# Kernel optimization log

Hardware: AMD Instinct MI355X
Metric: run time of the kernel (lower is better)

The kernel has to match this reference:

```python
import jax, jax.numpy as jnp
import numpy as np

B, N, DIM, H, POS_DIM = 8, 1024, 512, 8, 50
D = DIM // H


def setup_inputs() -> dict:
    key = jax.random.key(0)
    ks = jax.random.split(key, 7)
    s = 0.02
    return {
        "x": jax.random.normal(ks[0], (B, N, DIM), jnp.float32),
        "pos": jax.random.normal(ks[1], (1, N, N, POS_DIM), jnp.float32),
        "W_kv": jax.random.normal(ks[2], (2 * DIM, DIM), jnp.float32) * s,
        "W_out": jax.random.normal(ks[3], (DIM, DIM), jnp.float32) * s,
        "b_out": jax.random.normal(ks[4], (DIM,), jnp.float32) * s,
        "w_pos": jax.random.normal(ks[5], (POS_DIM,), jnp.float32) * s,
        "b_pos": jax.random.normal(ks[6], (1,), jnp.float32) * s,
    }


def reference(x, pos, W_kv, W_out, b_out, w_pos, b_pos):
    b, n, dim = x.shape
    h, d = H, dim // H
    scale = dim ** -0.5
    # to_kv: Linear(dim, 2*dim, bias=False); layout 'b n (kv h d)'
    kv = x @ W_kv.T                                   # (b, n, 2*dim)
    k = kv[..., :dim].reshape(b, n, h, d).transpose(0, 2, 1, 3)   # (b,h,n,d)
    v = kv[..., dim:].reshape(b, n, h, d).transpose(0, 2, 1, 3)   # (b,h,n,d)
    dots = jnp.einsum('bhid,bhjd->bhij', k, k) * scale            # (b,h,n,n)
    # map_pos(dots[...,None] + pos[None]) == dots*sum(w) + pos@w + bias (Linear is linear)
    pos_bias = jnp.einsum('ijp,p->ij', pos[0, :n, :n, :], w_pos)  # (n,n)
    scores = dots * jnp.sum(w_pos) + pos_bias + b_pos[0]
    attn = jax.nn.softmax(scores, axis=-1)
    out = jnp.einsum('bhij,bhjd->bhid', attn, v)                  # (b,h,n,d)
    out = out.transpose(0, 2, 1, 3).reshape(b, n, dim)            # (b,n,dim)
    return out @ W_out.T + b_out
```

## Files before the change

### kernel.cpp

```cpp
#include <hip/hip_runtime.h>

#define B_ 8
#define N_ 1024
#define DIM_ 512
#define H_ 8
#define D_ 64
#define PD_ 50
#define PBROWS 256

typedef __attribute__((ext_vector_type(4))) float f32x4;
typedef __attribute__((ext_vector_type(8))) __bf16 bf16x8;

__device__ __forceinline__ unsigned short f2bf(float f) {
    unsigned int u = __float_as_uint(f);
    u += 0x7FFFu + ((u >> 16) & 1u);
    return (unsigned short)(u >> 16);
}

__global__ __launch_bounds__(256) void cast_all(const float* __restrict__ x,
                                                const float* __restrict__ wkv,
                                                const float* __restrict__ wout,
                                                unsigned short* __restrict__ xb,
                                                unsigned short* __restrict__ wkvb,
                                                unsigned short* __restrict__ woutb) {
    const int bid = blockIdx.x;
    const float* src;
    unsigned short* dst;
    int idx;
    if (bid < 4096)      { src = x;    dst = xb;    idx = bid; }
    else if (bid < 4608) { src = wkv;  dst = wkvb;  idx = bid - 4096; }
    else                 { src = wout; dst = woutb; idx = bid - 4608; }
    int i = idx * 256 + threadIdx.x;
    float4 v = reinterpret_cast<const float4*>(src)[i];
    ushort4 o;
    o.x = f2bf(v.x); o.y = f2bf(v.y); o.z = f2bf(v.z); o.w = f2bf(v.w);
    reinterpret_cast<ushort4*>(dst)[i] = o;
}

__global__ __launch_bounds__(256) void pos_bias_kernel(const float* __restrict__ pos,
                                                       const float* __restrict__ w_pos,
                                                       float* __restrict__ pb) {
    __shared__ float buf[PBROWS * PD_];
    const int t = threadIdx.x;
    const size_t base = (size_t)blockIdx.x * (PBROWS * PD_);
    const float4* src = reinterpret_cast<const float4*>(pos + base);
    float4* dst = reinterpret_cast<float4*>(buf);
#pragma unroll 4
    for (int i = t; i < PBROWS * PD_ / 4; i += 256)
        dst[i] = src[i];
    __syncthreads();
    float acc = 0.f;
    const float* row = buf + t * PD_;
#pragma unroll
    for (int p = 0; p < PD_; p++) acc += row[p] * w_pos[p];
    pb[(size_t)blockIdx.x * PBROWS + t] = acc;
}

__global__ __launch_bounds__(256) void kv_gemm(const unsigned short* __restrict__ xb,
                                               const unsigned short* __restrict__ wb,
                                               unsigned short* __restrict__ kb,
                                               unsigned short* __restrict__ vt) {
    __shared__ __align__(16) unsigned short As[128][40];
    __shared__ __align__(16) unsigned short Bs[64][40];
    const int m0 = blockIdx.x * 128;
    const int n0 = blockIdx.y * 64;
    const int t = threadIdx.x;
    const int w = t >> 6, l = t & 63;
    const int wr = (w >> 1) * 64, wc = (w & 1) * 32;
    const int lr = l & 15, lg = l >> 4;
    const int ar = t >> 1, ac = (t & 1) * 16;
    const int br = t >> 2, bc = (t & 3) * 8;

    f32x4 acc[4][2] = {};

    for (int k0 = 0; k0 < DIM_; k0 += 32) {
        __syncthreads();
        *reinterpret_cast<bf16x8*>(&As[ar][ac]) =
            *reinterpret_cast<const bf16x8*>(&xb[(size_t)(m0 + ar) * DIM_ + k0 + ac]);
        *reinterpret_cast<bf16x8*>(&As[ar][ac + 8]) =
            *reinterpret_cast<const bf16x8*>(&xb[(size_t)(m0 + ar) * DIM_ + k0 + ac + 8]);
        *reinterpret_cast<bf16x8*>(&Bs[br][bc]) =
            *reinterpret_cast<const bf16x8*>(&wb[(size_t)(n0 + br) * DIM_ + k0 + bc]);
        __syncthreads();
        bf16x8 b0 = *reinterpret_cast<const bf16x8*>(&Bs[wc + lr][lg * 8]);
        bf16x8 b1 = *reinterpret_cast<const bf16x8*>(&Bs[wc + 16 + lr][lg * 8]);
#pragma unroll
        for (int fm = 0; fm < 4; fm++) {
            bf16x8 a = *reinterpret_cast<const bf16x8*>(&As[wr + fm * 16 + lr][lg * 8]);
            acc[fm][0] = __builtin_amdgcn_mfma_f32_16x16x32_bf16(a, b0, acc[fm][0], 0, 0, 0);
            acc[fm][1] = __builtin_amdgcn_mfma_f32_16x16x32_bf16(a, b1, acc[fm][1], 0, 0, 0);
        }
    }

#pragma unroll
    for (int fm = 0; fm < 4; fm++)
#pragma unroll
        for (int fn = 0; fn < 2; fn++) {
            int gn = n0 + wc + fn * 16 + lr;
#pragma unroll
            for (int i = 0; i < 4; i++) {
                int gm = m0 + wr + fm * 16 + lg * 4 + i;
                unsigned short bv = f2bf(acc[fm][fn][i]);
                int b = gm >> 10, nseq = gm & 1023;
                if (gn < DIM_) {
                    int h = gn >> 6, d = gn & 63;
                    kb[(((size_t)(b * H_ + h) * N_) + nseq) * D_ + d] = bv;
                } else {
                    int c = gn - DIM_;
                    int h = c >> 6, d = c & 63;
                    vt[(((size_t)(b * H_ + h) * D_) + d) * N_ + nseq] = bv;
                }
            }
        }
}

__global__ __launch_bounds__(256) void attn_kernel(const unsigned short* __restrict__ kb,
                                                   const unsigned short* __restrict__ vt,
                                                   const float* __restrict__ pb,
                                                   const float* __restrict__ w_pos,
                                                   unsigned short* __restrict__ oh) {
    const int bh = blockIdx.x;
    const int qt = blockIdx.y;
    const int b = bh >> 3, h = bh & 7;
    __shared__ __align__(16) unsigned short Qs[64][72];
    __shared__ __align__(16) unsigned short Ks[64][72];
    __shared__ __align__(16) unsigned short Vs[64][72];
    __shared__ __align__(16) unsigned short Ps[4][16][72];
    const int t = threadIdx.x, w = t >> 6, l = t & 63, lr = l & 15, lg = l >> 4;

    float sw = 0.f;
    for (int p = 0; p < PD_; p++) sw += w_pos[p];
    const float alpha = sw * 0.044194173824159216f;

    const unsigned short* kh = kb + (size_t)bh * N_ * D_;
    const unsigned short* vh = vt + (size_t)bh * D_ * N_;
    const int q0 = qt * 64;
    const int sr = t >> 2, sk = (t & 3) * 8;

    *reinterpret_cast<bf16x8*>(&Qs[sr][sk]) =
        *reinterpret_cast<const bf16x8*>(&kh[(size_t)(q0 + sr) * D_ + sk]);
    *reinterpret_cast<bf16x8*>(&Qs[sr][sk + 32]) =
        *reinterpret_cast<const bf16x8*>(&kh[(size_t)(q0 + sr) * D_ + sk + 32]);
    asm volatile("" ::: "memory");
    const bf16x8 aq0 = *reinterpret_cast<const bf16x8*>(&Qs[w * 16 + lr][lg * 8]);
    const bf16x8 aq1 = *reinterpret_cast<const bf16x8*>(&Qs[w * 16 + lr][32 + lg * 8]);

    float l_run[4] = {0.f, 0.f, 0.f, 0.f};
    f32x4 acc[4] = {};

    for (int jt = 0; jt < 16; jt++) {
        const int j0 = jt * 64;
        __syncthreads();
        *reinterpret_cast<bf16x8*>(&Ks[sr][sk]) =
            *reinterpret_cast<const bf16x8*>(&kh[(size_t)(j0 + sr) * D_ + sk]);
        *reinterpret_cast<bf16x8*>(&Ks[sr][sk + 32]) =
            *reinterpret_cast<const bf16x8*>(&kh[(size_t)(j0 + sr) * D_ + sk + 32]);
        *reinterpret_cast<bf16x8*>(&Vs[sr][sk]) =
            *reinterpret_cast<const bf16x8*>(&vh[(size_t)sr * N_ + j0 + sk]);
        *reinterpret_cast<bf16x8*>(&Vs[sr][sk + 32]) =
            *reinterpret_cast<const bf16x8*>(&vh[(size_t)sr * N_ + j0 + sk + 32]);
        __syncthreads();

        f32x4 s[4] = {};
#pragma unroll
        for (int fn = 0; fn < 4; fn++) {
            bf16x8 bk0 = *reinterpret_cast<const bf16x8*>(&Ks[fn * 16 + lr][lg * 8]);
            bf16x8 bk1 = *reinterpret_cast<const bf16x8*>(&Ks[fn * 16 + lr][32 + lg * 8]);
            s[fn] = __builtin_amdgcn_mfma_f32_16x16x32_bf16(aq0, bk0, s[fn], 0, 0, 0);
            s[fn] = __builtin_amdgcn_mfma_f32_16x16x32_bf16(aq1, bk1, s[fn], 0, 0, 0);
        }

#pragma unroll
        for (int fn = 0; fn < 4; fn++) {
            int gj = j0 + fn * 16 + lr;
#pragma unroll
            for (int i = 0; i < 4; i++) {
                int gq = q0 + w * 16 + lg * 4 + i;
                float p = __expf(s[fn][i] * alpha + pb[(size_t)gq * N_ + gj]);
                l_run[i] += p;
                Ps[w][lg * 4 + i][fn * 16 + lr] = f2bf(p);
            }
        }

        asm volatile("" ::: "memory");

        bf16x8 pa0 = *reinterpret_cast<const bf16x8*>(&Ps[w][lr][lg * 8]);
        bf16x8 pa1 = *reinterpret_cast<const bf16x8*>(&Ps[w][lr][32 + lg * 8]);
#pragma unroll
        for (int fd = 0; fd < 4; fd++) {
            bf16x8 bv0 = *reinterpret_cast<const bf16x8*>(&Vs[fd * 16 + lr][lg * 8]);
            bf16x8 bv1 = *reinterpret_cast<const bf16x8*>(&Vs[fd * 16 + lr][32 + lg * 8]);
            acc[fd] = __builtin_amdgcn_mfma_f32_16x16x32_bf16(pa0, bv0, acc[fd], 0, 0, 0);
            acc[fd] = __builtin_amdgcn_mfma_f32_16x16x32_bf16(pa1, bv1, acc[fd], 0, 0, 0);
        }
    }

#pragma unroll
    for (int msk = 1; msk < 16; msk <<= 1)
#pragma unroll
        for (int i = 0; i < 4; i++) l_run[i] += __shfl_xor(l_run[i], msk);

#pragma unroll
    for (int fd = 0; fd < 4; fd++) {
        int dcol = h * 64 + fd * 16 + lr;
#pragma unroll
        for (int i = 0; i < 4; i++) {
            int gq = q0 + w * 16 + lg * 4 + i;
            oh[((size_t)(b * N_ + gq)) * DIM_ + dcol] = f2bf(acc[fd][i] / l_run[i]);
        }
    }
}

__global__ __launch_bounds__(256) void out_gemm(const unsigned short* __restrict__ ohb,
                                                const unsigned short* __restrict__ wob,
                                                const float* __restrict__ b_out,
                                                float* __restrict__ out) {
    __shared__ __align__(16) unsigned short As[128][40];
    __shared__ __align__(16) unsigned short Bs[64][40];
    const int m0 = blockIdx.x * 128;
    const int n0 = blockIdx.y * 64;
    const int t = threadIdx.x;
    const int w = t >> 6, l = t & 63;
    const int wr = (w >> 1) * 64, wc = (w & 1) * 32;
    const int lr = l & 15, lg = l >> 4;
    const int ar = t >> 1, ac = (t & 1) * 16;
    const int br = t >> 2, bc = (t & 3) * 8;

    f32x4 acc[4][2] = {};

    for (int k0 = 0; k0 < DIM_; k0 += 32) {
        __syncthreads();
        *reinterpret_cast<bf16x8*>(&As[ar][ac]) =
            *reinterpret_cast<const bf16x8*>(&ohb[(size_t)(m0 + ar) * DIM_ + k0 + ac]);
        *reinterpret_cast<bf16x8*>(&As[ar][ac + 8]) =
            *reinterpret_cast<const bf16x8*>(&ohb[(size_t)(m0 + ar) * DIM_ + k0 + ac + 8]);
        *reinterpret_cast<bf16x8*>(&Bs[br][bc]) =
            *reinterpret_cast<const bf16x8*>(&wob[(size_t)(n0 + br) * DIM_ + k0 + bc]);
        __syncthreads();
        bf16x8 b0 = *reinterpret_cast<const bf16x8*>(&Bs[wc + lr][lg * 8]);
        bf16x8 b1 = *reinterpret_cast<const bf16x8*>(&Bs[wc + 16 + lr][lg * 8]);
#pragma unroll
        for (int fm = 0; fm < 4; fm++) {
            bf16x8 a = *reinterpret_cast<const bf16x8*>(&As[wr + fm * 16 + lr][lg * 8]);
            acc[fm][0] = __builtin_amdgcn_mfma_f32_16x16x32_bf16(a, b0, acc[fm][0], 0, 0, 0);
            acc[fm][1] = __builtin_amdgcn_mfma_f32_16x16x32_bf16(a, b1, acc[fm][1], 0, 0, 0);
        }
    }

#pragma unroll
    for (int fm = 0; fm < 4; fm++)
#pragma unroll
        for (int fn = 0; fn < 2; fn++) {
            int gn = n0 + wc + fn * 16 + lr;
            float bias = b_out[gn];
#pragma unroll
            for (int i = 0; i < 4; i++) {
                int gm = m0 + wr + fm * 16 + lg * 4 + i;
                out[(size_t)gm * DIM_ + gn] = acc[fm][fn][i] + bias;
            }
        }
}

extern "C" void kernel_launch(void* const* d_in, const int* in_sizes, int n_in,
                              void* d_out, int out_size, void* d_ws, size_t ws_size,
                              hipStream_t stream) {
    const float* x     = (const float*)d_in[0];
    const float* pos   = (const float*)d_in[1];
    const float* W_kv  = (const float*)d_in[2];
    const float* W_out = (const float*)d_in[3];
    const float* b_out = (const float*)d_in[4];
    const float* w_pos = (const float*)d_in[5];

    char* ws = (char*)d_ws;
    unsigned short* xb   = (unsigned short*)(ws);
    unsigned short* wkv  = (unsigned short*)(ws + 8388608);
    unsigned short* wout = (unsigned short*)(ws + 9437184);
    unsigned short* kb   = (unsigned short*)(ws + 9961472);
    unsigned short* vt   = (unsigned short*)(ws + 18350080);
    float*          pb   = (float*)(ws + 26738688);
    unsigned short* oh   = (unsigned short*)(ws + 30932992);
    float*          out  = (float*)d_out;

    cast_all<<<4864, 256, 0, stream>>>(x, W_kv, W_out, xb, wkv, wout);
    pos_bias_kernel<<<4096, 256, 0, stream>>>(pos, w_pos, pb);
    kv_gemm<<<dim3(64, 16), 256, 0, stream>>>(xb, wkv, kb, vt);
    attn_kernel<<<dim3(64, 16), 256, 0, stream>>>(kb, vt, pb, w_pos, oh);
    out_gemm<<<dim3(64, 8), 256, 0, stream>>>(oh, wout, b_out, out);
}
```

Measured before the change: 126.1 us.

## Process two query tiles per attention block with register-prefetched K/V; widen GEMM K-step

The attention kernel now handles 128 queries per block, as two 64-row halves that share each staged K/V tile. This halves K/V global traffic and the grid size. It also prefetches the next K/V tile into registers while the current tile is computed, and drops the separate Q shared buffer by staging Q through the K/V buffers. Both GEMM kernels now step K by 64 instead of 32, which halves the number of barrier-separated iterations. In exchange it needs more registers per thread, which may lower occupancy, and launches fewer attention blocks (512), which may underfill the GPU.

```diff
diff --git a/kernel.cpp b/kernel.cpp
--- a/kernel.cpp
+++ b/kernel.cpp
@@ -60,35 +60,40 @@
                                                const unsigned short* __restrict__ wb,
                                                unsigned short* __restrict__ kb,
                                                unsigned short* __restrict__ vt) {
-    __shared__ __align__(16) unsigned short As[128][40];
-    __shared__ __align__(16) unsigned short Bs[64][40];
+    __shared__ __align__(16) unsigned short As[128][72];
+    __shared__ __align__(16) unsigned short Bs[64][72];
     const int m0 = blockIdx.x * 128;
     const int n0 = blockIdx.y * 64;
     const int t = threadIdx.x;
     const int w = t >> 6, l = t & 63;
     const int wr = (w >> 1) * 64, wc = (w & 1) * 32;
     const int lr = l & 15, lg = l >> 4;
-    const int ar = t >> 1, ac = (t & 1) * 16;
-    const int br = t >> 2, bc = (t & 3) * 8;
+    const int ar = t >> 1, ac = (t & 1) * 32;
+    const int br = t >> 2, bc = (t & 3) * 16;
 
     f32x4 acc[4][2] = {};
 
-    for (int k0 = 0; k0 < DIM_; k0 += 32) {
-        __syncthreads();
-        *reinterpret_cast<bf16x8*>(&As[ar][ac]) =
-            *reinterpret_cast<const bf16x8*>(&xb[(size_t)(m0 + ar) * DIM_ + k0 + ac]);
-        *reinterpret_cast<bf16x8*>(&As[ar][ac + 8]) =
-            *reinterpret_cast<const bf16x8*>(&xb[(size_t)(m0 + ar) * DIM_ + k0 + ac + 8]);
-        *reinterpret_cast<bf16x8*>(&Bs[br][bc]) =
-            *reinterpret_cast<const bf16x8*>(&wb[(size_t)(n0 + br) * DIM_ + k0 + bc]);
-        __syncthreads();
-        bf16x8 b0 = *reinterpret_cast<const bf16x8*>(&Bs[wc + lr][lg * 8]);
-        bf16x8 b1 = *reinterpret_cast<const bf16x8*>(&Bs[wc + 16 + lr][lg * 8]);
-#pragma unroll
-        for (int fm = 0; fm < 4; fm++) {
-            bf16x8 a = *reinterpret_cast<const bf16x8*>(&As[wr + fm * 16 + lr][lg * 8]);
-            acc[fm][0] = __builtin_amdgcn_mfma_f32_16x16x32_bf16(a, b0, acc[fm][0], 0, 0, 0);
-            acc[fm][1] = __builtin_amdgcn_mfma_f32_16x16x32_bf16(a, b1, acc[fm][1], 0, 0, 0);
+    for (int k0 = 0; k0 < DIM_; k0 += 64) {
+        __syncthreads();
+#pragma unroll
+        for (int u = 0; u < 4; u++)
+            *reinterpret_cast<bf16x8*>(&As[ar][ac + u * 8]) =
+                *reinterpret_cast<const bf16x8*>(&xb[(size_t)(m0 + ar) * DIM_ + k0 + ac + u * 8]);
+#pragma unroll
+        for (int u = 0; u < 2; u++)
+            *reinterpret_cast<bf16x8*>(&Bs[br][bc + u * 8]) =
+                *reinterpret_cast<const bf16x8*>(&wb[(size_t)(n0 + br) * DIM_ + k0 + bc + u * 8]);
+        __syncthreads();
+#pragma unroll
+        for (int kh = 0; kh < 2; kh++) {
+            bf16x8 b0 = *reinterpret_cast<const bf16x8*>(&Bs[wc + lr][kh * 32 + lg * 8]);
+            bf16x8 b1 = *reinterpret_cast<const bf16x8*>(&Bs[wc + 16 + lr][kh * 32 + lg * 8]);
+#pragma unroll
+            for (int fm = 0; fm < 4; fm++) {
+                bf16x8 a = *reinterpret_cast<const bf16x8*>(&As[wr + fm * 16 + lr][kh * 32 + lg * 8]);
+                acc[fm][0] = __builtin_amdgcn_mfma_f32_16x16x32_bf16(a, b0, acc[fm][0], 0, 0, 0);
+                acc[fm][1] = __builtin_amdgcn_mfma_f32_16x16x32_bf16(a, b1, acc[fm][1], 0, 0, 0);
+            }
         }
     }
 
@@ -120,9 +125,8 @@
                                                    const float* __restrict__ w_pos,
                                                    unsigned short* __restrict__ oh) {
     const int bh = blockIdx.x;
-    const int qt = blockIdx.y;
+    const int qp = blockIdx.y;
     const int b = bh >> 3, h = bh & 7;
-    __shared__ __align__(16) unsigned short Qs[64][72];
     __shared__ __align__(16) unsigned short Ks[64][72];
     __shared__ __align__(16) unsigned short Vs[64][72];
     __shared__ __align__(16) unsigned short Ps[4][16][72];
@@ -134,40 +138,70 @@
 
     const unsigned short* kh = kb + (size_t)bh * N_ * D_;
     const unsigned short* vh = vt + (size_t)bh * D_ * N_;
-    const int q0 = qt * 64;
+    const int q0 = qp * 128;
     const int sr = t >> 2, sk = (t & 3) * 8;
 
-    *reinterpret_cast<bf16x8*>(&Qs[sr][sk]) =
+    *reinterpret_cast<bf16x8*>(&Ks[sr][sk]) =
         *reinterpret_cast<const bf16x8*>(&kh[(size_t)(q0 + sr) * D_ + sk]);
-    *reinterpret_cast<bf16x8*>(&Qs[sr][sk + 32]) =
+    *reinterpret_cast<bf16x8*>(&Ks[sr][sk + 32]) =
         *reinterpret_cast<const bf16x8*>(&kh[(size_t)(q0 + sr) * D_ + sk + 32]);
-    asm volatile("" ::: "memory");
-    const bf16x8 aq0 = *reinterpret_cast<const bf16x8*>(&Qs[w * 16 + lr][lg * 8]);
-    const bf16x8 aq1 = *reinterpret_cast<const bf16x8*>(&Qs[w * 16 + lr][32 + lg * 8]);
-
-    float l_run[4] = {0.f, 0.f, 0.f, 0.f};
-    f32x4 acc[4] = {};
+    *reinterpret_cast<bf16x8*>(&Vs[sr][sk]) =
+        *reinterpret_cast<const bf16x8*>(&kh[(size_t)(q0 + 64 + sr) * D_ + sk]);
+    *reinterpret_cast<bf16x8*>(&Vs[sr][sk + 32]) =
+        *reinterpret_cast<const bf16x8*>(&kh[(size_t)(q0 + 64 + sr) * D_ + sk + 32]);
+    __syncthreads();
+    const bf16x8 aqA0 = *reinterpret_cast<const bf16x8*>(&Ks[w * 16 + lr][lg * 8]);
+    const bf16x8 aqA1 = *reinterpret_cast<const bf16x8*>(&Ks[w * 16 + lr][32 + lg * 8]);
+    const bf16x8 aqB0 = *reinterpret_cast<const bf16x8*>(&Vs[w * 16 + lr][lg * 8]);
+    const bf16x8 aqB1 = *reinterpret_cast<const bf16x8*>(&Vs[w * 16 + lr][32 + lg * 8]);
+    __syncthreads();
+
+    *reinterpret_cast<bf16x8*>(&Ks[sr][sk]) =
+        *reinterpret_cast<const bf16x8*>(&kh[(size_t)sr * D_ + sk]);
+    *reinterpret_cast<bf16x8*>(&Ks[sr][sk + 32]) =
+        *reinterpret_cast<const bf16x8*>(&kh[(size_t)sr * D_ + sk + 32]);
+    *reinterpret_cast<bf16x8*>(&Vs[sr][sk]) =
+        *reinterpret_cast<const bf16x8*>(&vh[(size_t)sr * N_ + sk]);
+    *reinterpret_cast<bf16x8*>(&Vs[sr][sk + 32]) =
+        *reinterpret_cast<const bf16x8*>(&vh[(size_t)sr * N_ + sk + 32]);
+    __syncthreads();
+
+    float lA[4] = {0.f, 0.f, 0.f, 0.f}, lB[4] = {0.f, 0.f, 0.f, 0.f};
+    f32x4 accA[4] = {}, accB[4] = {};
 
     for (int jt = 0; jt < 16; jt++) {
         const int j0 = jt * 64;
-        __syncthreads();
-        *reinterpret_cast<bf16x8*>(&Ks[sr][sk]) =
-            *reinterpret_cast<const bf16x8*>(&kh[(size_t)(j0 + sr) * D_ + sk]);
-        *reinterpret_cast<bf16x8*>(&Ks[sr][sk + 32]) =
-            *reinterpret_cast<const bf16x8*>(&kh[(size_t)(j0 + sr) * D_ + sk + 32]);
-        *reinterpret_cast<bf16x8*>(&Vs[sr][sk]) =
-            *reinterpret_cast<const bf16x8*>(&vh[(size_t)sr * N_ + j0 + sk]);
-        *reinterpret_cast<bf16x8*>(&Vs[sr][sk + 32]) =
-            *reinterpret_cast<const bf16x8*>(&vh[(size_t)sr * N_ + j0 + sk + 32]);
-        __syncthreads();
-
-        f32x4 s[4] = {};
+
+        bf16x8 bk[4][2];
 #pragma unroll
         for (int fn = 0; fn < 4; fn++) {
-            bf16x8 bk0 = *reinterpret_cast<const bf16x8*>(&Ks[fn * 16 + lr][lg * 8]);
-            bf16x8 bk1 = *reinterpret_cast<const bf16x8*>(&Ks[fn * 16 + lr][32 + lg * 8]);
-            s[fn] = __builtin_amdgcn_mfma_f32_16x16x32_bf16(aq0, bk0, s[fn], 0, 0, 0);
-            s[fn] = __builtin_amdgcn_mfma_f32_16x16x32_bf16(aq1, bk1, s[fn], 0, 0, 0);
+            bk[fn][0] = *reinterpret_cast<const bf16x8*>(&Ks[fn * 16 + lr][lg * 8]);
+            bk[fn][1] = *reinterpret_cast<const bf16x8*>(&Ks[fn * 16 + lr][32 + lg * 8]);
+        }
+
+        bf16x8 rk0, rk1, rv0, rv1;
+        if (jt < 15) {
+            const int jn = j0 + 64;
+            rk0 = *reinterpret_cast<const bf16x8*>(&kh[(size_t)(jn + sr) * D_ + sk]);
+            rk1 = *reinterpret_cast<const bf16x8*>(&kh[(size_t)(jn + sr) * D_ + sk + 32]);
+            rv0 = *reinterpret_cast<const bf16x8*>(&vh[(size_t)sr * N_ + jn + sk]);
+            rv1 = *reinterpret_cast<const bf16x8*>(&vh[(size_t)sr * N_ + jn + sk + 32]);
+        }
+
+        f32x4 sA[4] = {}, sB[4] = {};
+#pragma unroll
+        for (int fn = 0; fn < 4; fn++) {
+            sA[fn] = __builtin_amdgcn_mfma_f32_16x16x32_bf16(aqA0, bk[fn][0], sA[fn], 0, 0, 0);
+            sA[fn] = __builtin_amdgcn_mfma_f32_16x16x32_bf16(aqA1, bk[fn][1], sA[fn], 0, 0, 0);
+            sB[fn] = __builtin_amdgcn_mfma_f32_16x16x32_bf16(aqB0, bk[fn][0], sB[fn], 0, 0, 0);
+            sB[fn] = __builtin_amdgcn_mfma_f32_16x16x32_bf16(aqB1, bk[fn][1], sB[fn], 0, 0, 0);
+        }
+
+        bf16x8 bv[4][2];
+#pragma unroll
+        for (int fd = 0; fd < 4; fd++) {
+            bv[fd][0] = *reinterpret_cast<const bf16x8*>(&Vs[fd * 16 + lr][lg * 8]);
+            bv[fd][1] = *reinterpret_cast<const bf16x8*>(&Vs[fd * 16 + lr][32 + lg * 8]);
         }
 
 #pragma unroll
@@ -176,37 +210,72 @@
 #pragma unroll
             for (int i = 0; i < 4; i++) {
                 int gq = q0 + w * 16 + lg * 4 + i;
-                float p = __expf(s[fn][i] * alpha + pb[(size_t)gq * N_ + gj]);
-                l_run[i] += p;
+                float p = __expf(sA[fn][i] * alpha + pb[(size_t)gq * N_ + gj]);
+                lA[i] += p;
                 Ps[w][lg * 4 + i][fn * 16 + lr] = f2bf(p);
             }
         }
-
         asm volatile("" ::: "memory");
-
-        bf16x8 pa0 = *reinterpret_cast<const bf16x8*>(&Ps[w][lr][lg * 8]);
-        bf16x8 pa1 = *reinterpret_cast<const bf16x8*>(&Ps[w][lr][32 + lg * 8]);
-#pragma unroll
-        for (int fd = 0; fd < 4; fd++) {
-            bf16x8 bv0 = *reinterpret_cast<const bf16x8*>(&Vs[fd * 16 + lr][lg * 8]);
-            bf16x8 bv1 = *reinterpret_cast<const bf16x8*>(&Vs[fd * 16 + lr][32 + lg * 8]);
-            acc[fd] = __builtin_amdgcn_mfma_f32_16x16x32_bf16(pa0, bv0, acc[fd], 0, 0, 0);
-            acc[fd] = __builtin_amdgcn_mfma_f32_16x16x32_bf16(pa1, bv1, acc[fd], 0, 0, 0);
-        }
+        {
+            bf16x8 pa0 = *reinterpret_cast<const bf16x8*>(&Ps[w][lr][lg * 8]);
+            bf16x8 pa1 = *reinterpret_cast<const bf16x8*>(&Ps[w][lr][32 + lg * 8]);
+#pragma unroll
+            for (int fd = 0; fd < 4; fd++) {
+                accA[fd] = __builtin_amdgcn_mfma_f32_16x16x32_bf16(pa0, bv[fd][0], accA[fd], 0, 0, 0);
+                accA[fd] = __builtin_amdgcn_mfma_f32_16x16x32_bf16(pa1, bv[fd][1], accA[fd], 0, 0, 0);
+            }
+        }
+        asm volatile("" ::: "memory");
+
+#pragma unroll
+        for (int fn = 0; fn < 4; fn++) {
+            int gj = j0 + fn * 16 + lr;
+#pragma unroll
+            for (int i = 0; i < 4; i++) {
+                int gq = q0 + 64 + w * 16 + lg * 4 + i;
+                float p = __expf(sB[fn][i] * alpha + pb[(size_t)gq * N_ + gj]);
+                lB[i] += p;
+                Ps[w][lg * 4 + i][fn * 16 + lr] = f2bf(p);
+            }
+        }
+        asm volatile("" ::: "memory");
+        {
+            bf16x8 pa0 = *reinterpret_cast<const bf16x8*>(&Ps[w][lr][lg * 8]);
+            bf16x8 pa1 = *reinterpret_cast<const bf16x8*>(&Ps[w][lr][32 + lg * 8]);
+#pragma unroll
+            for (int fd = 0; fd < 4; fd++) {
+                accB[fd] = __builtin_amdgcn_mfma_f32_16x16x32_bf16(pa0, bv[fd][0], accB[fd], 0, 0, 0);
+                accB[fd] = __builtin_amdgcn_mfma_f32_16x16x32_bf16(pa1, bv[fd][1], accB[fd], 0, 0, 0);
+            }
+        }
+
+        __syncthreads();
+        if (jt < 15) {
+            *reinterpret_cast<bf16x8*>(&Ks[sr][sk]) = rk0;
+            *reinterpret_cast<bf16x8*>(&Ks[sr][sk + 32]) = rk1;
+            *reinterpret_cast<bf16x8*>(&Vs[sr][sk]) = rv0;
+            *reinterpret_cast<bf16x8*>(&Vs[sr][sk + 32]) = rv1;
+        }
+        __syncthreads();
     }
 
 #pragma unroll
     for (int msk = 1; msk < 16; msk <<= 1)
 #pragma unroll
-        for (int i = 0; i < 4; i++) l_run[i] += __shfl_xor(l_run[i], msk);
+        for (int i = 0; i < 4; i++) {
+            lA[i] += __shfl_xor(lA[i], msk);
+            lB[i] += __shfl_xor(lB[i], msk);
+        }
 
 #pragma unroll
     for (int fd = 0; fd < 4; fd++) {
         int dcol = h * 64 + fd * 16 + lr;
 #pragma unroll
         for (int i = 0; i < 4; i++) {
-            int gq = q0 + w * 16 + lg * 4 + i;
-            oh[((size_t)(b * N_ + gq)) * DIM_ + dcol] = f2bf(acc[fd][i] / l_run[i]);
+            int gqA = q0 + w * 16 + lg * 4 + i;
+            oh[((size_t)(b * N_ + gqA)) * DIM_ + dcol] = f2bf(accA[fd][i] / lA[i]);
+            int gqB = gqA + 64;
+            oh[((size_t)(b * N_ + gqB)) * DIM_ + dcol] = f2bf(accB[fd][i] / lB[i]);
         }
     }
 }
@@ -215,35 +284,40 @@
                                                 const unsigned short* __restrict__ wob,
                                                 const float* __restrict__ b_out,
                                                 float* __restrict__ out) {
-    __shared__ __align__(16) unsigned short As[128][40];
-    __shared__ __align__(16) unsigned short Bs[64][40];
+    __shared__ __align__(16) unsigned short As[128][72];
+    __shared__ __align__(16) unsigned short Bs[64][72];
     const int m0 = blockIdx.x * 128;
     const int n0 = blockIdx.y * 64;
     const int t = threadIdx.x;
     const int w = t >> 6, l = t & 63;
     const int wr = (w >> 1) * 64, wc = (w & 1) * 32;
     const int lr = l & 15, lg = l >> 4;
-    const int ar = t >> 1, ac = (t & 1) * 16;
-    const int br = t >> 2, bc = (t & 3) * 8;
+    const int ar = t >> 1, ac = (t & 1) * 32;
+    const int br = t >> 2, bc = (t & 3) * 16;
 
     f32x4 acc[4][2] = {};
 
-    for (int k0 = 0; k0 < DIM_; k0 += 32) {
-        __syncthreads();
-        *reinterpret_cast<bf16x8*>(&As[ar][ac]) =
-            *reinterpret_cast<const bf16x8*>(&ohb[(size_t)(m0 + ar) * DIM_ + k0 + ac]);
-        *reinterpret_cast<bf16x8*>(&As[ar][ac + 8]) =
-            *reinterpret_cast<const bf16x8*>(&ohb[(size_t)(m0 + ar) * DIM_ + k0 + ac + 8]);
-        *reinterpret_cast<bf16x8*>(&Bs[br][bc]) =
-            *reinterpret_cast<const bf16x8*>(&wob[(size_t)(n0 + br) * DIM_ + k0 + bc]);
-        __syncthreads();
-        bf16x8 b0 = *reinterpret_cast<const bf16x8*>(&Bs[wc + lr][lg * 8]);
-        bf16x8 b1 = *reinterpret_cast<const bf16x8*>(&Bs[wc + 16 + lr][lg * 8]);
-#pragma unroll
-        for (int fm = 0; fm < 4; fm++) {
-            bf16x8 a = *reinterpret_cast<const bf16x8*>(&As[wr + fm * 16 + lr][lg * 8]);
-            acc[fm][0] = __builtin_amdgcn_mfma_f32_16x16x32_bf16(a, b0, acc[fm][0], 0, 0, 0);
-            acc[fm][1] = __builtin_amdgcn_mfma_f32_16x16x32_bf16(a, b1, acc[fm][1], 0, 0, 0);
+    for (int k0 = 0; k0 < DIM_; k0 += 64) {
+        __syncthreads();
+#pragma unroll
+        for (int u = 0; u < 4; u++)
+            *reinterpret_cast<bf16x8*>(&As[ar][ac + u * 8]) =
+                *reinterpret_cast<const bf16x8*>(&ohb[(size_t)(m0 + ar) * DIM_ + k0 + ac + u * 8]);
+#pragma unroll
+        for (int u = 0; u < 2; u++)
+            *reinterpret_cast<bf16x8*>(&Bs[br][bc + u * 8]) =
+                *reinterpret_cast<const bf16x8*>(&wob[(size_t)(n0 + br) * DIM_ + k0 + bc + u * 8]);
+        __syncthreads();
+#pragma unroll
+        for (int kh = 0; kh < 2; kh++) {
+            bf16x8 b0 = *reinterpret_cast<const bf16x8*>(&Bs[wc + lr][kh * 32 + lg * 8]);
+            bf16x8 b1 = *reinterpret_cast<const bf16x8*>(&Bs[wc + 16 + lr][kh * 32 + lg * 8]);
+#pragma unroll
+            for (int fm = 0; fm < 4; fm++) {
+                bf16x8 a = *reinterpret_cast<const bf16x8*>(&As[wr + fm * 16 + lr][kh * 32 + lg * 8]);
+                acc[fm][0] = __builtin_amdgcn_mfma_f32_16x16x32_bf16(a, b0, acc[fm][0], 0, 0, 0);
+                acc[fm][1] = __builtin_amdgcn_mfma_f32_16x16x32_bf16(a, b1, acc[fm][1], 0, 0, 0);
+            }
         }
     }
 
@@ -284,6 +358,6 @@
     cast_all<<<4864, 256, 0, stream>>>(x, W_kv, W_out, xb, wkv, wout);
     pos_bias_kernel<<<4096, 256, 0, stream>>>(pos, w_pos, pb);
     kv_gemm<<<dim3(64, 16), 256, 0, stream>>>(xb, wkv, kb, vt);
-    attn_kernel<<<dim3(64, 16), 256, 0, stream>>>(kb, vt, pb, w_pos, oh);
+    attn_kernel<<<dim3(64, 8), 256, 0, stream>>>(kb, vt, pb, w_pos, oh);
     out_gemm<<<dim3(64, 8), 256, 0, stream>>>(oh, wout, b_out, out);
 }
```

Result: faster. 120.5 us (median of 3 runs) (-4.5%).
